# Performance work log

Hardware: AMD Instinct MI355X
Metric: run time of the kernel (lower is better)

The kernel has to match this reference:

```python
import jax, jax.numpy as jnp
import numpy as np

KH, KW = 3, 3
H_OUT, W_OUT = 62, 62

def setup_inputs() -> dict:
    key = jax.random.key(0)
    k1, k2 = jax.random.split(key)
    x = jax.random.normal(k1, (16, 32, 64, 64), dtype=jnp.float32)
    weight = jax.random.normal(k2, (H_OUT, W_OUT, 64, 32, KH, KW), dtype=jnp.float32) * 0.01
    return {"x": x, "weight": weight}

def reference(x, weight):
    # Unfold: patches[b,c,kh,kw,i,j] = x[b,c,i+kh,j+kw]; small fixed 3x3 loop is fine.
    patches = jnp.stack([
        jnp.stack([x[:, :, kh:kh + H_OUT, kw:kw + W_OUT] for kw in range(KW)], axis=2)
        for kh in range(KH)
    ], axis=2)  # [B, C_in, kH, kW, H_out, W_out]
    # Per-position (no weight sharing) contraction over c_in, kh, kw.
    out = jnp.einsum('bcklij,ijockl->boij', patches, weight)
    return jax.nn.sigmoid(out)
```

## Files before the change

kernel.cpp:

```cpp
#include <hip/hip_runtime.h>

#define HO 62
#define WO 62
#define CIN 32
#define COUT 64
#define BATCH 16
#define KROW 288
#define NJT 31
#define NXCD 8

typedef float f4w __attribute__((ext_vector_type(4), aligned(16)));
typedef float f4x __attribute__((ext_vector_type(4), aligned(8)));

#define WSEL(arr, idx) (arr[(idx) >> 2][(idx) & 3])

__global__ __launch_bounds__(64, 2)
void lc2d_kernel(const float* __restrict__ x,
                 const float* __restrict__ wgt,
                 float* __restrict__ out) {
    const int orig = blockIdx.x;
    const int nwg  = HO * NJT;
    const int qch  = nwg / NXCD, rch = nwg % NXCD;
    const int xcd  = orig % NXCD, cpos = orig / NXCD;
    const int wg   = ((xcd < rch) ? xcd * (qch + 1)
                                  : rch * (qch + 1) + (xcd - rch) * qch) + cpos;
    const int i  = wg / NJT;
    const int j0 = (wg % NJT) * 2;
    const int pj = i * WO + j0;

    const int o = threadIdx.x;

    const float* w0 = wgt + ((size_t)pj * COUT + o) * KROW;
    const float* w1 = w0 + (size_t)COUT * KROW;

    const float* xb[BATCH];
    #pragma unroll
    for (int b = 0; b < BATCH; ++b) xb[b] = x + (size_t)b * (CIN * 64 * 64);

    float a0[BATCH], a1[BATCH];
    #pragma unroll
    for (int b = 0; b < BATCH; ++b) { a0[b] = 0.0f; a1[b] = 0.0f; }

    for (int ch = 0; ch < 8; ++ch) {
        f4w wa[9], wb[9];
        #pragma unroll
        for (int q = 0; q < 9; ++q) {
            wa[q] = *(const f4w*)(w0 + ch * 36 + q * 4);
            wb[q] = *(const f4w*)(w1 + ch * 36 + q * 4);
        }
        #pragma unroll
        for (int cc = 0; cc < 4; ++cc) {
            #pragma unroll
            for (int kh = 0; kh < 3; ++kh) {
                const int off = (((ch * 4 + cc) * 64) + i + kh) * 64 + j0;
                const int kb  = cc * 9 + kh * 3;
                #pragma unroll
                for (int b = 0; b < BATCH; ++b) {
                    const f4x xv = *(const f4x*)(xb[b] + off);
                    a0[b] += WSEL(wa, kb + 0) * xv.x;
                    a0[b] += WSEL(wa, kb + 1) * xv.y;
                    a0[b] += WSEL(wa, kb + 2) * xv.z;
                    a1[b] += WSEL(wb, kb + 0) * xv.y;
                    a1[b] += WSEL(wb, kb + 1) * xv.z;
                    a1[b] += WSEL(wb, kb + 2) * xv.w;
                }
            }
        }
    }

    #pragma unroll
    for (int b = 0; b < BATCH; ++b) {
        float* op = out + (size_t)(b * COUT + o) * (HO * WO) + pj;
        float2 s;
        s.x = 1.0f / (1.0f + __expf(-a0[b]));
        s.y = 1.0f / (1.0f + __expf(-a1[b]));
        *(float2*)op = s;
    }
}

extern "C" void kernel_launch(void* const* d_in, const int* in_sizes, int n_in,
                              void* d_out, int out_size, void* d_ws, size_t ws_size,
                              hipStream_t stream) {
    const float* x   = (const float*)d_in[0];
    const float* wgt = (const float*)d_in[1];
    float* out       = (float*)d_out;
    const int grid = HO * NJT;
    lc2d_kernel<<<dim3(grid), dim3(64), 0, stream>>>(x, wgt, out);
}
```

Baseline: 556.3 us.

## Stage weights via async global-to-LDS double buffering with 256-thread blocks

Each block now runs four waves, each covering one output position and half of the output channels with 8 batches per lane. Weight rows are copied into per-wave LDS slabs with global_load_lds in a double-buffered pipeline over eight input-channel phases, using manual vmcnt waits. The intent is to coalesce the strided per-thread weight reads, overlap them with compute, and raise occupancy by cutting registers per thread. The costs are unaligned x vector loads, a duplicated FMA path selected per position, and dependence on a hand-counted vmcnt value matching the number of outstanding loads.

Measured after the change: 1.016 ms. 82.6% more time.

```diff
diff --git a/kernel.cpp b/kernel.cpp
--- a/kernel.cpp
+++ b/kernel.cpp
@@ -2,22 +2,29 @@
 
 #define HO 62
 #define WO 62
+#define HW 3844
 #define CIN 32
 #define COUT 64
-#define BATCH 16
 #define KROW 288
 #define NJT 31
+#define NPH 8
+#define PHDW 36
+#define SLABDW 1152
 #define NXCD 8
 
-typedef float f4w __attribute__((ext_vector_type(4), aligned(16)));
-typedef float f4x __attribute__((ext_vector_type(4), aligned(8)));
+typedef const __attribute__((address_space(1))) void* gp_t;
+typedef __attribute__((address_space(3))) void* lp_t;
+typedef float f4   __attribute__((ext_vector_type(4)));
+typedef float f4a4 __attribute__((ext_vector_type(4), aligned(4)));
 
-#define WSEL(arr, idx) (arr[(idx) >> 2][(idx) & 3])
+#define WF(k) wf[(k) >> 2][(k) & 3]
 
-__global__ __launch_bounds__(64, 2)
+__global__ __launch_bounds__(256, 4)
 void lc2d_kernel(const float* __restrict__ x,
                  const float* __restrict__ wgt,
                  float* __restrict__ out) {
+    __shared__ __align__(16) float lds[4][2][SLABDW];
+
     const int orig = blockIdx.x;
     const int nwg  = HO * NJT;
     const int qch  = nwg / NXCD, rch = nwg % NXCD;
@@ -26,55 +33,119 @@
                                   : rch * (qch + 1) + (xcd - rch) * qch) + cpos;
     const int i  = wg / NJT;
     const int j0 = (wg % NJT) * 2;
-    const int pj = i * WO + j0;
 
-    const int o = threadIdx.x;
+    const int t      = threadIdx.x;
+    const int w      = t >> 6;
+    const int lane   = t & 63;
+    const int o5     = lane & 31;
+    const int bh     = lane >> 5;
+    const int posoff = w >> 1;
+    const int ohalf  = w & 1;
+    const int wsu    = __builtin_amdgcn_readfirstlane(w);
+    const int pj     = i * WO + j0 + posoff;
+    const int o      = ohalf * 32 + o5;
 
-    const float* w0 = wgt + ((size_t)pj * COUT + o) * KROW;
-    const float* w1 = w0 + (size_t)COUT * KROW;
+    const float* S = wgt + ((size_t)pj * COUT + ohalf * 32) * KROW;
 
-    const float* xb[BATCH];
+    int g16[4], g4[2];
     #pragma unroll
-    for (int b = 0; b < BATCH; ++b) xb[b] = x + (size_t)b * (CIN * 64 * 64);
+    for (int q = 0; q < 4; ++q) {
+        const int U = q * 64 + lane;
+        g16[q] = (U / 9) * KROW + (U % 9) * 4;
+    }
+    #pragma unroll
+    for (int q = 0; q < 2; ++q) {
+        const int d = 1024 + q * 64 + lane;
+        g4[q] = (d / PHDW) * KROW + (d % PHDW);
+    }
 
-    float a0[BATCH], a1[BATCH];
+    float* const lbase = &lds[wsu][0][0];
+
+    const float* xq[8];
     #pragma unroll
-    for (int b = 0; b < BATCH; ++b) { a0[b] = 0.0f; a1[b] = 0.0f; }
+    for (int bi = 0; bi < 8; ++bi)
+        xq[bi] = x + (size_t)(bh * 8 + bi) * (CIN * 4096) + i * 64 + j0;
 
-    for (int ch = 0; ch < 8; ++ch) {
-        f4w wa[9], wb[9];
+    float acc[8];
+    #pragma unroll
+    for (int bi = 0; bi < 8; ++bi) acc[bi] = 0.0f;
+
+    #pragma unroll
+    for (int q = 0; q < 4; ++q)
+        __builtin_amdgcn_global_load_lds((gp_t)(S + g16[q]), (lp_t)(lbase + q * 256), 16, 0, 0);
+    #pragma unroll
+    for (int q = 0; q < 2; ++q)
+        __builtin_amdgcn_global_load_lds((gp_t)(S + g4[q]), (lp_t)(lbase + 1024 + q * 64), 4, 0, 0);
+
+    const float* wsrc = S + PHDW;
+    int cur = 0;
+    int xph = 0;
+
+    #pragma unroll 1
+    for (int p = 0; p < NPH; ++p) {
+        __builtin_amdgcn_sched_barrier(0);
+        if (p + 1 < NPH) {
+            float* nb = lbase + (cur ^ 1) * SLABDW;
+            #pragma unroll
+            for (int q = 0; q < 4; ++q)
+                __builtin_amdgcn_global_load_lds((gp_t)(wsrc + g16[q]), (lp_t)(nb + q * 256), 16, 0, 0);
+            #pragma unroll
+            for (int q = 0; q < 2; ++q)
+                __builtin_amdgcn_global_load_lds((gp_t)(wsrc + g4[q]), (lp_t)(nb + 1024 + q * 64), 4, 0, 0);
+            wsrc += PHDW;
+        }
+        __builtin_amdgcn_sched_barrier(0);
+        if (p + 1 < NPH) { asm volatile("s_waitcnt vmcnt(6)" ::: "memory"); }
+        else             { asm volatile("s_waitcnt vmcnt(0)" ::: "memory"); }
+        __builtin_amdgcn_sched_barrier(0);
+
+        const float* wb = lbase + cur * SLABDW + o5 * PHDW;
+        f4 wf[9];
         #pragma unroll
-        for (int q = 0; q < 9; ++q) {
-            wa[q] = *(const f4w*)(w0 + ch * 36 + q * 4);
-            wb[q] = *(const f4w*)(w1 + ch * 36 + q * 4);
-        }
-        #pragma unroll
-        for (int cc = 0; cc < 4; ++cc) {
+        for (int g = 0; g < 9; ++g)
+            wf[g] = *(const f4*)(wb + g * 4);
+
+        if (posoff == 0) {
             #pragma unroll
-            for (int kh = 0; kh < 3; ++kh) {
-                const int off = (((ch * 4 + cc) * 64) + i + kh) * 64 + j0;
-                const int kb  = cc * 9 + kh * 3;
+            for (int cc = 0; cc < 4; ++cc) {
                 #pragma unroll
-                for (int b = 0; b < BATCH; ++b) {
-                    const f4x xv = *(const f4x*)(xb[b] + off);
-                    a0[b] += WSEL(wa, kb + 0) * xv.x;
-                    a0[b] += WSEL(wa, kb + 1) * xv.y;
-                    a0[b] += WSEL(wa, kb + 2) * xv.z;
-                    a1[b] += WSEL(wb, kb + 0) * xv.y;
-                    a1[b] += WSEL(wb, kb + 1) * xv.z;
-                    a1[b] += WSEL(wb, kb + 2) * xv.w;
+                for (int kh = 0; kh < 3; ++kh) {
+                    const int xoff = xph + cc * 4096 + kh * 64;
+                    const int k0 = cc * 9 + kh * 3;
+                    #pragma unroll
+                    for (int bi = 0; bi < 8; ++bi) {
+                        const f4a4 xv = *(const f4a4*)(xq[bi] + xoff);
+                        acc[bi] += WF(k0 + 0) * xv.x;
+                        acc[bi] += WF(k0 + 1) * xv.y;
+                        acc[bi] += WF(k0 + 2) * xv.z;
+                    }
+                }
+            }
+        } else {
+            #pragma unroll
+            for (int cc = 0; cc < 4; ++cc) {
+                #pragma unroll
+                for (int kh = 0; kh < 3; ++kh) {
+                    const int xoff = xph + cc * 4096 + kh * 64;
+                    const int k0 = cc * 9 + kh * 3;
+                    #pragma unroll
+                    for (int bi = 0; bi < 8; ++bi) {
+                        const f4a4 xv = *(const f4a4*)(xq[bi] + xoff);
+                        acc[bi] += WF(k0 + 0) * xv.y;
+                        acc[bi] += WF(k0 + 1) * xv.z;
+                        acc[bi] += WF(k0 + 2) * xv.w;
+                    }
                 }
             }
         }
+        xph += 4 * 4096;
+        cur ^= 1;
     }
 
     #pragma unroll
-    for (int b = 0; b < BATCH; ++b) {
-        float* op = out + (size_t)(b * COUT + o) * (HO * WO) + pj;
-        float2 s;
-        s.x = 1.0f / (1.0f + __expf(-a0[b]));
-        s.y = 1.0f / (1.0f + __expf(-a1[b]));
-        *(float2*)op = s;
+    for (int bi = 0; bi < 8; ++bi) {
+        const int b = bh * 8 + bi;
+        out[(size_t)(b * COUT + o) * HW + pj] = 1.0f / (1.0f + __expf(-acc[bi]));
     }
 }
 
@@ -85,5 +156,5 @@
     const float* wgt = (const float*)d_in[1];
     float* out       = (float*)d_out;
     const int grid = HO * NJT;
-    lc2d_kernel<<<dim3(grid), dim3(64), 0, stream>>>(x, wgt, out);
+    lc2d_kernel<<<dim3(grid), dim3(256), 0, stream>>>(x, wgt, out);
 }
```
